# Optimization experiments

Hardware: AMD Instinct MI355X
Metric: run time of the kernel (lower is better)

## Reference

```python
import jax, jax.numpy as jnp
import numpy as np

N_NODES = 50000
N_EDGES = 800000
D_IN = 128
D_OUT = 128


def setup_inputs() -> dict:
    key = jax.random.key(0)
    k1, k2, k3, k4 = jax.random.split(key, 4)
    X = jax.random.normal(k1, (N_NODES, D_IN), dtype=jnp.float32)
    weight = jax.random.normal(k2, (D_IN, D_OUT), dtype=jnp.float32) * (1.0 / np.sqrt(D_OUT))
    edge_src = jax.random.randint(k3, (N_EDGES,), 0, N_NODES, dtype=jnp.int32)
    edge_dst = jax.random.randint(k4, (N_EDGES,), 0, N_NODES, dtype=jnp.int32)
    return {"X": X, "weight": weight, "edge_src": edge_src, "edge_dst": edge_dst}


def reference(X, weight, edge_src, edge_dst):
    # GCN: out = A_hat_hat @ (X @ W), A_hat_hat = D^-1/2 (A + I) D^-1/2
    ones = jnp.ones((edge_src.shape[0],), dtype=X.dtype)
    # node degrees (+1 for implicit self loop, avoids div-by-zero)
    deg = jax.ops.segment_sum(ones, edge_dst, num_segments=N_NODES) + 1.0
    inv_sqrt_deg = jax.lax.rsqrt(deg)  # [N]
    XW = X @ weight  # [N, D_OUT] dense GEMM
    # per-edge normalization 1/sqrt(d_i * d_j)
    norm = inv_sqrt_deg[edge_dst] * inv_sqrt_deg[edge_src]  # [E]
    msg = XW[edge_src] * norm[:, None]  # [E, D_OUT] gather
    agg = jax.ops.segment_sum(msg, edge_dst, num_segments=N_NODES)  # scatter-add
    # self-loop contribution: 1/d_i * XW[i]
    out = agg + XW * (inv_sqrt_deg * inv_sqrt_deg)[:, None]
    return out
```

## Files before the change

kernel.cpp:

```cpp
#include <hip/hip_runtime.h>

#define N_NODES 50000
#define N_EDGES 800000
#define D 128

#define NBLK 250
#define EPB (N_EDGES / NBLK)
#define NQ (EPB / 4)
#define NBKT 196
#define CAP 6144

typedef __attribute__((ext_vector_type(8))) short bf16x8;
typedef __attribute__((ext_vector_type(4))) float f32x4;

static const size_t OFF_TOT  = 0;
static const size_t OFF_WT   = 1024;
static const size_t OFF_H    = 33792;
static const size_t OFF_BB   = 234496;
static const size_t OFF_DEG  = 435200;
static const size_t OFF_OFFS = 635200;
static const size_t OFF_IVS  = 835200;
static const size_t OFF_REC  = 1235200;
static const size_t OFF_CSR  = 6052096;
static const size_t OFF_XWQ  = 8460544;

#define BM 64
#define NB_GEMM ((N_NODES + BM - 1) / BM)

__device__ __forceinline__ unsigned short f2bf(float f) {
    unsigned int u = __float_as_uint(f);
    unsigned int r = (u + 0x7fffu + ((u >> 16) & 1u)) >> 16;
    return (unsigned short)r;
}
__device__ __forceinline__ float sb(unsigned int u, int i) {
    return (float)((int)(u << (24 - 8 * i)) >> 24);
}

__global__ __launch_bounds__(256) void k_pre(const int* __restrict__ dst,
                                             int* __restrict__ H,
                                             const float* __restrict__ W,
                                             unsigned short* __restrict__ Wt) {
    __shared__ unsigned int cnt[256];
    int bid = blockIdx.x, t = threadIdx.x;
    if (bid >= NBLK) {
        int idx = (bid - NBLK) * 256 + t;
        int n = idx >> 7, k = idx & 127;
        Wt[n * D + k] = f2bf(W[k * D + n]);
        return;
    }
    cnt[t] = 0;
    __syncthreads();
    int e0 = bid * EPB;
    for (int q = t; q < NQ; q += 256) {
        int4 d4 = *(const int4*)&dst[e0 + q * 4];
        atomicAdd(&cnt[d4.x >> 8], 1u);
        atomicAdd(&cnt[d4.y >> 8], 1u);
        atomicAdd(&cnt[d4.z >> 8], 1u);
        atomicAdd(&cnt[d4.w >> 8], 1u);
    }
    __syncthreads();
    if (t < NBKT) H[t * 256 + bid] = (int)cnt[t];
}

__global__ __launch_bounds__(256) void k_pB(const int* __restrict__ H,
                                            int* __restrict__ BB,
                                            int* __restrict__ TOT) {
    int k = blockIdx.x, t = threadIdx.x;
    int w = t >> 6, l = t & 63;
    int v = (t < NBLK) ? H[k * 256 + t] : 0;
    int s = v;
    #pragma unroll
    for (int d = 1; d < 64; d <<= 1) {
        int u = __shfl_up(s, d, 64);
        if (l >= d) s += u;
    }
    __shared__ int wtot[4], woff[4];
    if (l == 63) wtot[w] = s;
    __syncthreads();
    if (t == 0) {
        woff[0] = 0; woff[1] = wtot[0];
        woff[2] = wtot[0] + wtot[1]; woff[3] = wtot[0] + wtot[1] + wtot[2];
    }
    __syncthreads();
    int excl = s - v + woff[w];
    BB[k * 256 + t] = excl;
    if (t == 255) TOT[k] = excl + v;
}

__global__ __launch_bounds__(512) void k_pC(const int* __restrict__ src,
                                            const int* __restrict__ dst,
                                            const int* __restrict__ BB,
                                            unsigned int* __restrict__ rec) {
    __shared__ unsigned int cnt[200];
    __shared__ int myBB[NBKT];
    int b = blockIdx.x, t = threadIdx.x;
    if (t < 200) cnt[t] = 0;
    if (t < NBKT) myBB[t] = t * CAP + BB[t * 256 + b];
    __syncthreads();
    int e0 = b * EPB;
    for (int q = t; q < NQ; q += 512) {
        int4 d4 = *(const int4*)&dst[e0 + q * 4];
        int4 s4 = *(const int4*)&src[e0 + q * 4];
        {
            int k = d4.x >> 8;
            unsigned int r = atomicAdd(&cnt[k], 1u);
            rec[myBB[k] + (int)r] = (unsigned int)s4.x | ((unsigned int)(d4.x & 255) << 16);
        }
        {
            int k = d4.y >> 8;
            unsigned int r = atomicAdd(&cnt[k], 1u);
            rec[myBB[k] + (int)r] = (unsigned int)s4.y | ((unsigned int)(d4.y & 255) << 16);
        }
        {
            int k = d4.z >> 8;
            unsigned int r = atomicAdd(&cnt[k], 1u);
            rec[myBB[k] + (int)r] = (unsigned int)s4.z | ((unsigned int)(d4.z & 255) << 16);
        }
        {
            int k = d4.w >> 8;
            unsigned int r = atomicAdd(&cnt[k], 1u);
            rec[myBB[k] + (int)r] = (unsigned int)s4.w | ((unsigned int)(d4.w & 255) << 16);
        }
    }
}

__global__ __launch_bounds__(256) void k_mid(const unsigned int* __restrict__ rec,
                                             const int* __restrict__ TOT,
                                             int* __restrict__ deg,
                                             int* __restrict__ offs,
                                             float* __restrict__ ivs,
                                             unsigned short* __restrict__ csr,
                                             const float* __restrict__ X,
                                             const unsigned short* __restrict__ Wt,
                                             char* __restrict__ XWq) {
    __shared__ unsigned short sA[BM * D];
    __shared__ unsigned short sB[D * D];
    __shared__ int wtot[4], woff[4];
    int bid = blockIdx.x;
    int t = threadIdx.x;
    int w = t >> 6, l = t & 63;

    if (bid >= NBKT) {
        int r0 = (bid - NBKT) * BM;

        #pragma unroll
        for (int p = 0; p < 8; ++p) {
            int e = p * 2048 + t * 8;
            int n = e >> 7, k = e & 127;
            uint4 v = *(const uint4*)&Wt[e];
            int idx = n * D + (((k >> 3) ^ (n & 7)) << 3);
            *(uint4*)&sB[idx] = v;
        }
        #pragma unroll
        for (int p = 0; p < 8; ++p) {
            int e = p * 1024 + t * 4;
            int r = e >> 7, c = e & 127;
            int row = r0 + r;
            float4 xv = make_float4(0.f, 0.f, 0.f, 0.f);
            if (row < N_NODES) xv = *(const float4*)&X[row * D + c];
            ushort4 bv;
            bv.x = f2bf(xv.x); bv.y = f2bf(xv.y); bv.z = f2bf(xv.z); bv.w = f2bf(xv.w);
            int idx = r * D + (((c >> 3) ^ (r & 7)) << 3) + (c & 7);
            *(ushort4*)&sA[idx] = bv;
        }
        __syncthreads();

        int arow = w * 16 + (l & 15);
        f32x4 acc[8];
        #pragma unroll
        for (int i = 0; i < 8; ++i) acc[i] = (f32x4){0.f, 0.f, 0.f, 0.f};

        #pragma unroll
        for (int kk = 0; kk < 4; ++kk) {
            int g = kk * 4 + (l >> 4);
            bf16x8 a = *(bf16x8*)&sA[arow * D + ((g ^ (arow & 7)) << 3)];
            #pragma unroll
            for (int nt = 0; nt < 8; ++nt) {
                int nrow = nt * 16 + (l & 15);
                bf16x8 b = *(bf16x8*)&sB[nrow * D + ((g ^ (nrow & 7)) << 3)];
                acc[nt] = __builtin_amdgcn_mfma_f32_16x16x32_bf16(a, b, acc[nt], 0, 0, 0);
            }
        }

        float rmax[4];
        #pragma unroll
        for (int r = 0; r < 4; ++r) {
            float m = 0.f;
            #pragma unroll
            for (int nt = 0; nt < 8; ++nt) m = fmaxf(m, fabsf(acc[nt][r]));
            #pragma unroll
            for (int d = 1; d < 16; d <<= 1) m = fmaxf(m, __shfl_xor(m, d, 64));
            rmax[r] = fmaxf(m, 1e-20f);
        }

        __syncthreads();
        char* sQ = (char*)sA;
        #pragma unroll
        for (int r = 0; r < 4; ++r) {
            float qs = 127.0f / rmax[r];
            int row = w * 16 + (l >> 4) * 4 + r;
            #pragma unroll
            for (int nt = 0; nt < 8; ++nt) {
                float f = acc[nt][r] * qs;
                f = fminf(fmaxf(f, -127.0f), 127.0f);
                sQ[row * D + nt * 16 + (l & 15)] = (char)__float2int_rn(f);
            }
            if ((l & 15) == 0) {
                int m = r0 + row;
                if (m < N_NODES) ivs[m * 2 + 1] = rmax[r] * (1.0f / 127.0f);
            }
        }
        __syncthreads();

        int limit = (N_NODES - r0) * D;
        if (limit > BM * D) limit = BM * D;
        const uint4* q4 = (const uint4*)sQ;
        uint4* dst4 = (uint4*)(XWq + (size_t)r0 * D);
        if (t * 16 < limit) dst4[t] = q4[t];
        if ((t + 256) * 16 < limit) dst4[t + 256] = q4[t + 256];
        return;
    }

    unsigned int* lcnt = (unsigned int*)sA;
    int* off_l = ((int*)sA) + 256;
    int k = bid;
    int base = k * CAP;
    int tot = TOT[k];

    lcnt[t] = 0;
    __syncthreads();
    for (int i = t; i < tot; i += 256)
        atomicAdd(&lcnt[rec[base + i] >> 16], 1u);
    __syncthreads();

    int v = (int)lcnt[t];
    int vr = (v + 3) & ~3;
    int s = vr;
    #pragma unroll
    for (int d = 1; d < 64; d <<= 1) {
        int u = __shfl_up(s, d, 64);
        if (l >= d) s += u;
    }
    if (l == 63) wtot[w] = s;
    __syncthreads();
    if (t == 0) {
        woff[0] = 0; woff[1] = wtot[0];
        woff[2] = wtot[0] + wtot[1]; woff[3] = wtot[0] + wtot[1] + wtot[2];
    }
    __syncthreads();
    int excl = s - vr + woff[w];
    off_l[t] = excl;
    int node = k * 256 + t;
    if (node < N_NODES) {
        deg[node] = v;
        ivs[node * 2] = rsqrtf((float)v + 1.0f);
        offs[node] = base + excl;
    }
    for (int j = v; j < vr; ++j) csr[base + excl + j] = 0;
    __syncthreads();
    lcnt[t] = 0;
    __syncthreads();
    for (int i = t; i < tot; i += 256) {
        unsigned int rc = rec[base + i];
        int dl = rc >> 16;
        unsigned int r = atomicAdd(&lcnt[dl], 1u);
        csr[base + off_l[dl] + (int)r] = (unsigned short)(rc & 0xFFFFu);
    }
}

__global__ __launch_bounds__(256) void k_agg(const char* __restrict__ XWq,
                                             const float2* __restrict__ ivs,
                                             const unsigned short* __restrict__ csr,
                                             const int* __restrict__ offs,
                                             const int* __restrict__ deg,
                                             float* __restrict__ out) {
    __shared__ int s_off[16];
    __shared__ int s_cnt[16];
    __shared__ float2 s_iv[16];
    int n0 = blockIdx.x * 16;
    int t = threadIdx.x;
    if (t < 16) {
        int n = n0 + t;
        int ok = (n < N_NODES);
        s_off[t] = ok ? offs[n] : 0;
        s_cnt[t] = ok ? deg[n] : -1;
        s_iv[t] = ok ? ivs[n] : make_float2(0.f, 0.f);
    }
    __syncthreads();
    int li = t >> 4;
    int cl = t & 15;
    int node = n0 + li;
    int cnt = s_cnt[li];
    if (cnt < 0) return;
    int start = s_off[li];
    float2 vs = s_iv[li];
    float invd = vs.x;

    float acc[8];
    {
        float sc = invd * invd * vs.y;
        uint2 v = *(const uint2*)&XWq[(size_t)node * D + cl * 8];
        acc[0] = sc * sb(v.x, 0); acc[1] = sc * sb(v.x, 1);
        acc[2] = sc * sb(v.x, 2); acc[3] = sc * sb(v.x, 3);
        acc[4] = sc * sb(v.y, 0); acc[5] = sc * sb(v.y, 1);
        acc[6] = sc * sb(v.y, 2); acc[7] = sc * sb(v.y, 3);
    }

    for (int e = 0; e < cnt; e += 8) {
        uint2 ca = *(const uint2*)&csr[start + e];
        uint2 cb = *(const uint2*)&csr[start + e + 4];
        int si[8];
        si[0] = ca.x & 0xffff; si[1] = ca.x >> 16;
        si[2] = ca.y & 0xffff; si[3] = ca.y >> 16;
        si[4] = cb.x & 0xffff; si[5] = cb.x >> 16;
        si[6] = cb.y & 0xffff; si[7] = cb.y >> 16;
        uint2 v[8];
        float nn[8];
        #pragma unroll
        for (int u = 0; u < 8; ++u) {
            v[u] = *(const uint2*)&XWq[(size_t)si[u] * D + cl * 8];
            float2 iv = ivs[si[u]];
            nn[u] = (e + u < cnt) ? invd * iv.x * iv.y : 0.f;
        }
        #pragma unroll
        for (int u = 0; u < 8; ++u) {
            float n = nn[u];
            acc[0] += n * sb(v[u].x, 0); acc[1] += n * sb(v[u].x, 1);
            acc[2] += n * sb(v[u].x, 2); acc[3] += n * sb(v[u].x, 3);
            acc[4] += n * sb(v[u].y, 0); acc[5] += n * sb(v[u].y, 1);
            acc[6] += n * sb(v[u].y, 2); acc[7] += n * sb(v[u].y, 3);
        }
    }

    float4 o0 = make_float4(acc[0], acc[1], acc[2], acc[3]);
    float4 o1 = make_float4(acc[4], acc[5], acc[6], acc[7]);
    *(float4*)&out[node * D + cl * 8] = o0;
    *(float4*)&out[node * D + cl * 8 + 4] = o1;
}

extern "C" void kernel_launch(void* const* d_in, const int* in_sizes, int n_in,
                              void* d_out, int out_size, void* d_ws, size_t ws_size,
                              hipStream_t stream) {
    const float* X = (const float*)d_in[0];
    const float* W = (const float*)d_in[1];
    const int* esrc = (const int*)d_in[2];
    const int* edst = (const int*)d_in[3];
    float* out = (float*)d_out;

    char* ws = (char*)d_ws;
    int* TOT = (int*)(ws + OFF_TOT);
    unsigned short* Wt = (unsigned short*)(ws + OFF_WT);
    int* H = (int*)(ws + OFF_H);
    int* BB = (int*)(ws + OFF_BB);
    int* deg = (int*)(ws + OFF_DEG);
    int* offs = (int*)(ws + OFF_OFFS);
    float* ivs = (float*)(ws + OFF_IVS);
    unsigned int* rec = (unsigned int*)(ws + OFF_REC);
    unsigned short* csr = (unsigned short*)(ws + OFF_CSR);
    char* XWq = (char*)(ws + OFF_XWQ);

    k_pre<<<NBLK + 64, 256, 0, stream>>>(edst, H, W, Wt);
    k_pB<<<NBKT, 256, 0, stream>>>(H, BB, TOT);
    k_pC<<<NBLK, 512, 0, stream>>>(esrc, edst, BB, rec);
    k_mid<<<NBKT + NB_GEMM, 256, 0, stream>>>(rec, TOT, deg, offs, ivs, csr,
                                              X, Wt, XWq);
    k_agg<<<(N_NODES + 15) / 16, 256, 0, stream>>>(XWq, (const float2*)ivs, csr,
                                                   offs, deg, out);
}
```

Measured before the change: 62.27 us.

## Load GEMM A-operand from global directly and drop LDS staging for XWq

The GEMM blocks in k_mid now read X rows from global memory straight into MFMA A registers, converting to bf16 in registers instead of staging through an LDS tile. The quantized int8 output is written byte-wise straight to global rather than through LDS and a coalesced uint4 copy, which removes two barriers and the sA buffer and so lowers LDS use per block. The final output stores become nontemporal. The cost is less coalesced global reads of X and scattered byte-wide global writes of XWq.

```diff
diff --git a/kernel.cpp b/kernel.cpp
--- a/kernel.cpp
+++ b/kernel.cpp
@@ -133,7 +133,6 @@
                                              const float* __restrict__ X,
                                              const unsigned short* __restrict__ Wt,
                                              char* __restrict__ XWq) {
-    __shared__ unsigned short sA[BM * D];
     __shared__ unsigned short sB[D * D];
     __shared__ int wtot[4], woff[4];
     int bid = blockIdx.x;
@@ -151,21 +150,11 @@
             int idx = n * D + (((k >> 3) ^ (n & 7)) << 3);
             *(uint4*)&sB[idx] = v;
         }
-        #pragma unroll
-        for (int p = 0; p < 8; ++p) {
-            int e = p * 1024 + t * 4;
-            int r = e >> 7, c = e & 127;
-            int row = r0 + r;
-            float4 xv = make_float4(0.f, 0.f, 0.f, 0.f);
-            if (row < N_NODES) xv = *(const float4*)&X[row * D + c];
-            ushort4 bv;
-            bv.x = f2bf(xv.x); bv.y = f2bf(xv.y); bv.z = f2bf(xv.z); bv.w = f2bf(xv.w);
-            int idx = r * D + (((c >> 3) ^ (r & 7)) << 3) + (c & 7);
-            *(ushort4*)&sA[idx] = bv;
-        }
         __syncthreads();
 
         int arow = w * 16 + (l & 15);
+        int xrow = r0 + arow;
+        bool okr = (xrow < N_NODES);
         f32x4 acc[8];
         #pragma unroll
         for (int i = 0; i < 8; ++i) acc[i] = (f32x4){0.f, 0.f, 0.f, 0.f};
@@ -173,7 +162,17 @@
         #pragma unroll
         for (int kk = 0; kk < 4; ++kk) {
             int g = kk * 4 + (l >> 4);
-            bf16x8 a = *(bf16x8*)&sA[arow * D + ((g ^ (arow & 7)) << 3)];
+            float4 xa = make_float4(0.f, 0.f, 0.f, 0.f);
+            float4 xb = make_float4(0.f, 0.f, 0.f, 0.f);
+            if (okr) {
+                xa = *(const float4*)&X[xrow * D + g * 8];
+                xb = *(const float4*)&X[xrow * D + g * 8 + 4];
+            }
+            bf16x8 a;
+            a[0] = (short)f2bf(xa.x); a[1] = (short)f2bf(xa.y);
+            a[2] = (short)f2bf(xa.z); a[3] = (short)f2bf(xa.w);
+            a[4] = (short)f2bf(xb.x); a[5] = (short)f2bf(xb.y);
+            a[6] = (short)f2bf(xb.z); a[7] = (short)f2bf(xb.w);
             #pragma unroll
             for (int nt = 0; nt < 8; ++nt) {
                 int nrow = nt * 16 + (l & 15);
@@ -193,36 +192,30 @@
             rmax[r] = fmaxf(m, 1e-20f);
         }
 
-        __syncthreads();
-        char* sQ = (char*)sA;
         #pragma unroll
         for (int r = 0; r < 4; ++r) {
             float qs = 127.0f / rmax[r];
             int row = w * 16 + (l >> 4) * 4 + r;
-            #pragma unroll
-            for (int nt = 0; nt < 8; ++nt) {
-                float f = acc[nt][r] * qs;
-                f = fminf(fmaxf(f, -127.0f), 127.0f);
-                sQ[row * D + nt * 16 + (l & 15)] = (char)__float2int_rn(f);
+            int m = r0 + row;
+            if (m < N_NODES) {
+                char q8[8];
+                #pragma unroll
+                for (int nt = 0; nt < 8; ++nt) {
+                    float f = acc[nt][r] * qs;
+                    f = fminf(fmaxf(f, -127.0f), 127.0f);
+                    q8[nt] = (char)__float2int_rn(f);
+                }
+                #pragma unroll
+                for (int nt = 0; nt < 8; ++nt)
+                    XWq[(size_t)m * D + nt * 16 + (l & 15)] = q8[nt];
+                if ((l & 15) == 0) ivs[m * 2 + 1] = rmax[r] * (1.0f / 127.0f);
             }
-            if ((l & 15) == 0) {
-                int m = r0 + row;
-                if (m < N_NODES) ivs[m * 2 + 1] = rmax[r] * (1.0f / 127.0f);
-            }
-        }
-        __syncthreads();
-
-        int limit = (N_NODES - r0) * D;
-        if (limit > BM * D) limit = BM * D;
-        const uint4* q4 = (const uint4*)sQ;
-        uint4* dst4 = (uint4*)(XWq + (size_t)r0 * D);
-        if (t * 16 < limit) dst4[t] = q4[t];
-        if ((t + 256) * 16 < limit) dst4[t + 256] = q4[t + 256];
+        }
         return;
     }
 
-    unsigned int* lcnt = (unsigned int*)sA;
-    int* off_l = ((int*)sA) + 256;
+    unsigned int* lcnt = (unsigned int*)sB;
+    int* off_l = ((int*)sB) + 256;
     int k = bid;
     int base = k * CAP;
     int tot = TOT[k];
@@ -332,10 +325,10 @@
         }
     }
 
-    float4 o0 = make_float4(acc[0], acc[1], acc[2], acc[3]);
-    float4 o1 = make_float4(acc[4], acc[5], acc[6], acc[7]);
-    *(float4*)&out[node * D + cl * 8] = o0;
-    *(float4*)&out[node * D + cl * 8 + 4] = o1;
+    f32x4 o0 = (f32x4){acc[0], acc[1], acc[2], acc[3]};
+    f32x4 o1 = (f32x4){acc[4], acc[5], acc[6], acc[7]};
+    __builtin_nontemporal_store(o0, (f32x4*)&out[node * D + cl * 8]);
+    __builtin_nontemporal_store(o1, (f32x4*)&out[node * D + cl * 8 + 4]);
 }
 
 extern "C" void kernel_launch(void* const* d_in, const int* in_sizes, int n_in,
```

New measurement: 61.62 us (median of 2 runs). No clear change (-1.1%).
